# Optimization experiments

Measured on AMD Instinct MI355X. Metric: run time of the kernel, lower is better.

The kernel has to match this reference:

```python
import jax, jax.numpy as jnp
import numpy as np

E = 2048
H = 16
HD = E // H
S = 2048
B = 2
SCALE = 1.0 / np.sqrt(HD)


def setup_inputs() -> dict:
    key = jax.random.key(0)
    ks = jax.random.split(key, 5)
    std = 1.0 / np.sqrt(E)
    return {
        "inX": jax.random.normal(ks[0], (B, S, E), dtype=jnp.float32),
        "W_qkv": jax.random.normal(ks[1], (E, 3 * E), dtype=jnp.float32) * std,
        "b_qkv": jax.random.normal(ks[2], (3 * E,), dtype=jnp.float32) * std,
        "W_out": jax.random.normal(ks[3], (E, E), dtype=jnp.float32) * std,
        "b_out": jax.random.normal(ks[4], (E,), dtype=jnp.float32) * std,
    }


def reference(inX, W_qkv, b_qkv, W_out, b_out):
    b, s, e = inX.shape
    qkv = inX @ W_qkv + b_qkv                      # [B,S,3E]
    q, k, v = jnp.split(qkv, 3, axis=2)
    # [B,S,H,HD] -> [B,H,S,HD]
    q = q.reshape(b, s, H, HD).transpose(0, 2, 1, 3)
    k = k.reshape(b, s, H, HD).transpose(0, 2, 1, 3)
    v = v.reshape(b, s, H, HD).transpose(0, 2, 1, 3)
    att = jnp.einsum("bhqd,bhkd->bhqk", q, k) * SCALE
    causal = jnp.tril(jnp.ones((s, s), dtype=bool))
    att = jnp.where(causal, att, -jnp.inf)
    att = jax.nn.softmax(att, axis=-1)
    out = jnp.einsum("bhqk,bhkd->bhqd", att, v)
    out = out.transpose(0, 2, 1, 3).reshape(b, s, e)
    return out @ W_out + b_out
```

## Files before the change

### kernel.cpp

```cpp
#include <hip/hip_runtime.h>


typedef unsigned short u16;
typedef unsigned int   u32;
typedef __attribute__((ext_vector_type(4)))  float f32x4;
typedef __attribute__((ext_vector_type(16))) float f32x16;
typedef __attribute__((ext_vector_type(4)))  unsigned int u32x4;
typedef __attribute__((ext_vector_type(4)))  unsigned short u16x4;
typedef __attribute__((ext_vector_type(8)))  short bf16x8;

#define E_    2048
#define H_    16
#define HD_   128
#define S_    2048
#define B_    2
#define M_    (B_ * S_)
#define N1_   (3 * E_)
static constexpr float SCALE = 0.08838834764831845f;
static constexpr float C2LOG = 0.12752224f;

__device__ __forceinline__ u16 f2bf(float f) {
  union { float f; u32 u; } x; x.f = f;
  u32 r = x.u + 0x7fffu + ((x.u >> 16) & 1u);
  return (u16)(r >> 16);
}
__device__ __forceinline__ float bfhi2f(u32 u) {
  union { u32 u; float f; } x; x.u = u & 0xffff0000u; return x.f;
}
__device__ __forceinline__ float bflo2f(u32 u) {
  union { u32 u; float f; } x; x.u = u << 16; return x.f;
}
__device__ __forceinline__ u32 pk2(float a, float b) {
  return (u32)f2bf(a) | ((u32)f2bf(b) << 16);
}

__global__ __launch_bounds__(256) void cvt_bf16(const float* __restrict__ x,
                                                u16* __restrict__ y, int n) {
  int i = (blockIdx.x * 256 + threadIdx.x) * 8;
  if (i >= n) return;
  f32x4 a = *(const f32x4*)(x + i);
  f32x4 b = *(const f32x4*)(x + i + 4);
  u16x4 u0 = { f2bf(a[0]), f2bf(a[1]), f2bf(a[2]), f2bf(a[3]) };
  u16x4 u1 = { f2bf(b[0]), f2bf(b[1]), f2bf(b[2]), f2bf(b[3]) };
  *(u16x4*)(y + i)     = u0;
  *(u16x4*)(y + i + 4) = u1;
}

__global__ __launch_bounds__(256) void transpose_cvt_f32(const float* __restrict__ W,
                                                         u16* __restrict__ Wt,
                                                         int rows, int cols) {
  __shared__ __align__(16) u16 tile[64][68];
  const int ct = blockIdx.x, rt = blockIdx.y;
  const int tid = threadIdx.x;
  const int seg = tid & 15, r0 = tid >> 4;
  for (int p = 0; p < 4; ++p) {
    int r = r0 + p * 16;
    f32x4 f = *(const f32x4*)&W[(size_t)(rt * 64 + r) * cols + ct * 64 + seg * 4];
    u16x4 u = { f2bf(f[0]), f2bf(f[1]), f2bf(f[2]), f2bf(f[3]) };
    *(u16x4*)&tile[r][seg * 4] = u;
  }
  __syncthreads();
  for (int p = 0; p < 4; ++p) {
    int oc = r0 + p * 16;
    u16x4 u = { tile[seg * 4 + 0][oc], tile[seg * 4 + 1][oc],
                tile[seg * 4 + 2][oc], tile[seg * 4 + 3][oc] };
    *(u16x4*)&Wt[(size_t)(ct * 64 + oc) * rows + rt * 64 + seg * 4] = u;
  }
}

__global__ __launch_bounds__(256) void transpose_v(const u16* __restrict__ qkv,
                                                   u16* __restrict__ vt) {
  __shared__ __align__(16) u16 tile[64][68];
  const int st = blockIdx.x;
  const int ct = blockIdx.y;
  const int tid = threadIdx.x;
  const int seg = tid & 15, r0 = tid >> 4;
  for (int p = 0; p < 4; ++p) {
    int r = r0 + p * 16;
    *(u16x4*)&tile[r][seg * 4] =
        *(const u16x4*)&qkv[(size_t)(st * 64 + r) * N1_ + 2 * E_ + ct * 64 + seg * 4];
  }
  __syncthreads();
  const int b = st >> 5, s0 = (st & 31) * 64;
  const int h = ct >> 1, d0 = (ct & 1) * 64;
  for (int p = 0; p < 4; ++p) {
    int oc = r0 + p * 16;
    u16x4 u = { tile[seg * 4 + 0][oc], tile[seg * 4 + 1][oc],
                tile[seg * 4 + 2][oc], tile[seg * 4 + 3][oc] };
    *(u16x4*)&vt[(size_t)((b * H_ + h) * HD_ + d0 + oc) * S_ + s0 + seg * 4] = u;
  }
}

template<int OUT_F32>
__global__ __launch_bounds__(256) void gemm_bt(const u16* __restrict__ A,
                                               const u16* __restrict__ Bt,
                                               const float* __restrict__ bias,
                                               void* __restrict__ Cp,
                                               int M, int N, int K) {
  const int bn = blockIdx.x, bm = blockIdx.y;
  const int tid = threadIdx.x;
  const int wid = tid >> 6, l = tid & 63;
  const int l15 = l & 15, l4 = l >> 4;
  const int wr = wid >> 1, wc = wid & 1;

  __shared__ __align__(16) u16 As[128 * 32];
  __shared__ __align__(16) u16 Bs[128 * 32];

  f32x4 acc[4][4] = {};

  const int lrow = l >> 2, lseg = l & 3;
  const u16* gA = A + (size_t)(bm * 128 + lrow) * K + lseg * 8;
  const u16* gB = Bt + (size_t)(bn * 128 + lrow) * K + lseg * 8;

  for (int kt = 0; kt < K; kt += 32) {
    for (int i = 0; i < 2; ++i) {
      int ch = wid * 2 + i;
      __builtin_amdgcn_global_load_lds(
          (__attribute__((address_space(1))) const void*)(gA + (size_t)(ch * 16) * K + kt),
          (__attribute__((address_space(3))) void*)(As + ch * 512), 16, 0, 0);
      __builtin_amdgcn_global_load_lds(
          (__attribute__((address_space(1))) const void*)(gB + (size_t)(ch * 16) * K + kt),
          (__attribute__((address_space(3))) void*)(Bs + ch * 512), 16, 0, 0);
    }
    __syncthreads();
    bf16x8 af[4], bfr[4];
    for (int i = 0; i < 4; ++i) {
      af[i]  = *(const bf16x8*)&As[(wr * 64 + i * 16 + l15) * 32 + l4 * 8];
      bfr[i] = *(const bf16x8*)&Bs[(wc * 64 + i * 16 + l15) * 32 + l4 * 8];
    }
    for (int mi = 0; mi < 4; ++mi)
      for (int ni = 0; ni < 4; ++ni)
        acc[mi][ni] = __builtin_amdgcn_mfma_f32_16x16x32_bf16(af[mi], bfr[ni],
                                                              acc[mi][ni], 0, 0, 0);
    __syncthreads();
  }

  for (int ni = 0; ni < 4; ++ni) {
    int col = bn * 128 + wc * 64 + ni * 16 + l15;
    float bs = bias[col];
    for (int mi = 0; mi < 4; ++mi) {
      int row = bm * 128 + wr * 64 + mi * 16 + l4 * 4;
      for (int j = 0; j < 4; ++j) {
        float v = acc[mi][ni][j] + bs;
        if (OUT_F32) ((float*)Cp)[(size_t)(row + j) * N + col] = v;
        else         ((u16*)Cp)[(size_t)(row + j) * N + col] = f2bf(v);
      }
    }
  }
}

__global__ __launch_bounds__(256) void attn3(const u16* __restrict__ qkv,
                                             const u16* __restrict__ vt,
                                             u16* __restrict__ outp) {
  const int i_lin = (int)blockIdx.x + 16 * (int)blockIdx.y;
  const int bh = i_lin & 31;
  const int h8 = i_lin >> 5;
  const int qt = (h8 < 8) ? h8 : 23 - h8;
  const int b = bh >> 4, h = bh & 15;
  const int tid = threadIdx.x;
  const int w = tid >> 6, l = tid & 63;
  const int l31 = l & 31, hi = l >> 5, l15 = l & 15, l4 = l >> 4;

  __shared__ __align__(16) u16 Ks[128 * 128];
  __shared__ __align__(16) u16 Vs[128 * 128];

  const int q_glob = qt * 128 + w * 32 + l31;
  const int qmin_w = qt * 128 + w * 32;
  const int qmax_w = qmin_w + 31;

  bf16x8 qf[8];
  {
    const u16* qrow = qkv + (size_t)(b * S_ + q_glob) * N1_ + h * HD_;
#pragma unroll
    for (int kd = 0; kd < 8; ++kd) {
      u32x4 raw = *(const u32x4*)(qrow + kd * 16 + hi * 8);
      u32x4 o;
#pragma unroll
      for (int j = 0; j < 4; ++j) {
        float flo = bflo2f(raw[j]) * C2LOG;
        float fhi = bfhi2f(raw[j]) * C2LOG;
        o[j] = (u32)f2bf(flo) | ((u32)f2bf(fhi) << 16);
      }
      union { u32x4 u; bf16x8 b; } cv; cv.u = o; qf[kd] = cv.b;
    }
  }

  int slotKe[8];
#pragma unroll
  for (int kd = 0; kd < 8; ++kd) slotKe[kd] = ((2 * kd + hi) ^ l15) * 8;

  f32x16 o0 = {}, o1 = {}, o2 = {}, o3 = {};
  float m_run = -1e30f, lsum = 0.f;

  const int pairs = qt + 1;
  for (int t = 0; t < pairs; ++t) {
    __syncthreads();
#pragma unroll
    for (int i = 0; i < 8; ++i) {
      const int rowbase = i * 16 + w * 4;
      const int r = rowbase + l4;
      const int e = (l15 ^ (r & 15)) * 8;
      __builtin_amdgcn_global_load_lds(
          (__attribute__((address_space(1))) const void*)
              (qkv + (size_t)(b * S_ + t * 128 + r) * N1_ + E_ + h * HD_ + e),
          (__attribute__((address_space(3))) void*)(Ks + rowbase * 128), 16, 0, 0);
      __builtin_amdgcn_global_load_lds(
          (__attribute__((address_space(1))) const void*)
              (vt + (size_t)(bh * HD_ + r) * S_ + t * 128 + e),
          (__attribute__((address_space(3))) void*)(Vs + rowbase * 128), 16, 0, 0);
    }
    asm volatile("s_waitcnt vmcnt(0)");
    __syncthreads();

#pragma unroll
    for (int p = 0; p < 2; ++p) {
      const int kbase = t * 128 + p * 64;
      if (kbase > qmax_w) continue;

      f32x16 sc0 = {}, sc1 = {};
#pragma unroll
      for (int kd = 0; kd < 8; ++kd) {
        bf16x8 ka0 = *(const bf16x8*)(Ks + (size_t)(p * 64 + l31) * 128 + slotKe[kd]);
        bf16x8 ka1 = *(const bf16x8*)(Ks + (size_t)(p * 64 + 32 + l31) * 128 + slotKe[kd]);
        sc0 = __builtin_amdgcn_mfma_f32_32x32x16_bf16(ka0, qf[kd], sc0, 0, 0, 0);
        sc1 = __builtin_amdgcn_mfma_f32_32x32x16_bf16(ka1, qf[kd], sc1, 0, 0, 0);
      }

      if (kbase + 63 > qmin_w) {
#pragma unroll
        for (int r = 0; r < 16; ++r) {
          int k0 = kbase + 8 * (r >> 2) + 4 * hi + (r & 3);
          if (k0 > q_glob)      sc0[r] = -1e30f;
          if (k0 + 32 > q_glob) sc1[r] = -1e30f;
        }
      }

      float tm = -1e30f;
#pragma unroll
      for (int r = 0; r < 16; ++r) tm = fmaxf(tm, fmaxf(sc0[r], sc1[r]));
      tm = fmaxf(tm, __shfl_xor(tm, 32));
      if (tm > m_run + 8.0f) {
        float alpha = exp2f(m_run - tm);
        m_run = tm;
        lsum *= alpha;
#pragma unroll
        for (int r = 0; r < 16; ++r) {
          o0[r] *= alpha; o1[r] *= alpha; o2[r] *= alpha; o3[r] *= alpha;
        }
      }
      float s0 = 0.f, s1 = 0.f;
#pragma unroll
      for (int r = 0; r < 16; ++r) {
        float p0 = exp2f(sc0[r] - m_run); sc0[r] = p0; s0 += p0;
        float p1 = exp2f(sc1[r] - m_run); sc1[r] = p1; s1 += p1;
      }
      lsum += s0 + s1;

      bf16x8 pf[4];
#pragma unroll
      for (int kd = 0; kd < 4; ++kd) {
        const f32x16& scf = (kd < 2) ? sc0 : sc1;
        const int rb = (kd & 1) * 8;
        u32 xa = pk2(scf[rb + 0], scf[rb + 1]);
        u32 ya = pk2(scf[rb + 2], scf[rb + 3]);
        u32 xb = pk2(scf[rb + 4], scf[rb + 5]);
        u32 yb = pk2(scf[rb + 6], scf[rb + 7]);
        u32 sxa = __shfl_xor(xa, 32), sya = __shfl_xor(ya, 32);
        u32 sxb = __shfl_xor(xb, 32), syb = __shfl_xor(yb, 32);
        u32x4 fw;
        fw[0] = hi ? sxb : xa;   fw[1] = hi ? syb : ya;
        fw[2] = hi ? xb  : sxa;  fw[3] = hi ? yb  : sya;
        union { u32x4 u; bf16x8 b; } cv; cv.u = fw; pf[kd] = cv.b;
      }

#pragma unroll
      for (int kd = 0; kd < 4; ++kd) {
        const int vofs = slotKe[kd] ^ (p * 64);
        bf16x8 va0 = *(const bf16x8*)(Vs + (size_t)(0  + l31) * 128 + vofs);
        bf16x8 va1 = *(const bf16x8*)(Vs + (size_t)(32 + l31) * 128 + vofs);
        bf16x8 va2 = *(const bf16x8*)(Vs + (size_t)(64 + l31) * 128 + vofs);
        bf16x8 va3 = *(const bf16x8*)(Vs + (size_t)(96 + l31) * 128 + vofs);
        o0 = __builtin_amdgcn_mfma_f32_32x32x16_bf16(va0, pf[kd], o0, 0, 0, 0);
        o1 = __builtin_amdgcn_mfma_f32_32x32x16_bf16(va1, pf[kd], o1, 0, 0, 0);
        o2 = __builtin_amdgcn_mfma_f32_32x32x16_bf16(va2, pf[kd], o2, 0, 0, 0);
        o3 = __builtin_amdgcn_mfma_f32_32x32x16_bf16(va3, pf[kd], o3, 0, 0, 0);
      }
    }
  }

  lsum += __shfl_xor(lsum, 32);
  const float inv = 1.0f / lsum;
  u16* orow = outp + (size_t)(b * S_ + q_glob) * E_ + h * HD_;
#pragma unroll
  for (int df = 0; df < 4; ++df) {
    const f32x16& oo = (df == 0) ? o0 : (df == 1) ? o1 : (df == 2) ? o2 : o3;
#pragma unroll
    for (int g = 0; g < 4; ++g) {
      int d = 32 * df + 8 * g + 4 * hi;
      u16x4 u = { f2bf(oo[g * 4 + 0] * inv), f2bf(oo[g * 4 + 1] * inv),
                  f2bf(oo[g * 4 + 2] * inv), f2bf(oo[g * 4 + 3] * inv) };
      *(u16x4*)(orow + d) = u;
    }
  }
}

extern "C" void kernel_launch(void* const* d_in, const int* in_sizes, int n_in,
                              void* d_out, int out_size, void* d_ws, size_t ws_size,
                              hipStream_t stream) {
  const float* inX  = (const float*)d_in[0];
  const float* Wqkv = (const float*)d_in[1];
  const float* bqkv = (const float*)d_in[2];
  const float* Wout = (const float*)d_in[3];
  const float* bout = (const float*)d_in[4];

  char* ws = (char*)d_ws;
  u16* Xb   = (u16*)(ws);
  u16* Wqt  = (u16*)(ws + (16u << 20));
  u16* Wot  = (u16*)(ws + (40u << 20));
  u16* QKV  = (u16*)(ws + (48u << 20));
  u16* Vt   = Wqt;
  u16* Attn = Xb;

  cvt_bf16<<<(M_ * E_) / (256 * 8), 256, 0, stream>>>(inX, Xb, M_ * E_);
  transpose_cvt_f32<<<dim3(N1_ / 64, E_ / 64), 256, 0, stream>>>(Wqkv, Wqt, E_, N1_);
  transpose_cvt_f32<<<dim3(E_ / 64, E_ / 64), 256, 0, stream>>>(Wout, Wot, E_, E_);
  gemm_bt<0><<<dim3(N1_ / 128, M_ / 128), 256, 0, stream>>>(Xb, Wqt, bqkv, (void*)QKV,
                                                            M_, N1_, E_);
  transpose_v<<<dim3(M_ / 64, E_ / 64), 256, 0, stream>>>(QKV, Vt);
  attn3<<<dim3(16, 32), 256, 0, stream>>>(QKV, Vt, Attn);
  gemm_bt<1><<<dim3(E_ / 128, M_ / 128), 256, 0, stream>>>(Attn, Wot, bout, d_out,
                                                           M_, E_, E_);
}
```

Measured before the change: 313.0 us.

## Double-buffer GEMM LDS tiles with BK=64 and XOR-swizzled layout

The bf16 GEMM kernel now uses two LDS buffers with a K-tile of 64 and prefetches the next tile through global_load_lds while MFMAs run on the current one, gated by an explicit vmcnt wait. The LDS layout is XOR-swizzled per row so the fragment reads avoid bank conflicts. The aim is to hide global-load latency and halve the number of barriers per K. In exchange, LDS use quadruples to 64KB per block, which may reduce occupancy, and correctness now depends on the hand-written vmcnt count.

```diff
diff --git a/kernel.cpp b/kernel.cpp
--- a/kernel.cpp
+++ b/kernel.cpp
@@ -103,35 +103,57 @@
   const int l15 = l & 15, l4 = l >> 4;
   const int wr = wid >> 1, wc = wid & 1;
 
-  __shared__ __align__(16) u16 As[128 * 32];
-  __shared__ __align__(16) u16 Bs[128 * 32];
+  __shared__ __align__(16) u16 As[2][128 * 64];
+  __shared__ __align__(16) u16 Bs[2][128 * 64];
 
   f32x4 acc[4][4] = {};
 
-  const int lrow = l >> 2, lseg = l & 3;
-  const u16* gA = A + (size_t)(bm * 128 + lrow) * K + lseg * 8;
-  const u16* gB = Bt + (size_t)(bn * 128 + lrow) * K + lseg * 8;
-
-  for (int kt = 0; kt < K; kt += 32) {
-    for (int i = 0; i < 2; ++i) {
-      int ch = wid * 2 + i;
+  const int srow  = l >> 3;
+  const int sslot = (l & 7) ^ srow;
+  const u16* gA = A  + (size_t)(bm * 128 + srow) * K + sslot * 8;
+  const u16* gB = Bt + (size_t)(bn * 128 + srow) * K + sslot * 8;
+
+  auto stage = [&](int buf, int kt) {
+#pragma unroll
+    for (int i = 0; i < 4; ++i) {
+      const int rb = i * 32 + wid * 8;
       __builtin_amdgcn_global_load_lds(
-          (__attribute__((address_space(1))) const void*)(gA + (size_t)(ch * 16) * K + kt),
-          (__attribute__((address_space(3))) void*)(As + ch * 512), 16, 0, 0);
+          (__attribute__((address_space(1))) const void*)(gA + (size_t)rb * K + kt),
+          (__attribute__((address_space(3))) void*)(&As[buf][rb * 64]), 16, 0, 0);
       __builtin_amdgcn_global_load_lds(
-          (__attribute__((address_space(1))) const void*)(gB + (size_t)(ch * 16) * K + kt),
-          (__attribute__((address_space(3))) void*)(Bs + ch * 512), 16, 0, 0);
+          (__attribute__((address_space(1))) const void*)(gB + (size_t)rb * K + kt),
+          (__attribute__((address_space(3))) void*)(&Bs[buf][rb * 64]), 16, 0, 0);
+    }
+  };
+
+  stage(0, 0);
+  const int nk = K >> 6;
+  for (int n = 0; n < nk; ++n) {
+    const int buf = n & 1;
+    if (n + 1 < nk) {
+      stage(buf ^ 1, (n + 1) << 6);
+      asm volatile("s_waitcnt vmcnt(8)" ::: "memory");
+    } else {
+      asm volatile("s_waitcnt vmcnt(0)" ::: "memory");
     }
     __syncthreads();
-    bf16x8 af[4], bfr[4];
-    for (int i = 0; i < 4; ++i) {
-      af[i]  = *(const bf16x8*)&As[(wr * 64 + i * 16 + l15) * 32 + l4 * 8];
-      bfr[i] = *(const bf16x8*)&Bs[(wc * 64 + i * 16 + l15) * 32 + l4 * 8];
-    }
-    for (int mi = 0; mi < 4; ++mi)
-      for (int ni = 0; ni < 4; ++ni)
-        acc[mi][ni] = __builtin_amdgcn_mfma_f32_16x16x32_bf16(af[mi], bfr[ni],
-                                                              acc[mi][ni], 0, 0, 0);
+
+#pragma unroll
+    for (int ks = 0; ks < 2; ++ks) {
+      bf16x8 af[4], bfr[4];
+      const int ph = ((ks * 4 + l4) ^ (l15 & 7)) * 8;
+#pragma unroll
+      for (int i = 0; i < 4; ++i) {
+        af[i]  = *(const bf16x8*)&As[buf][(wr * 64 + i * 16 + l15) * 64 + ph];
+        bfr[i] = *(const bf16x8*)&Bs[buf][(wc * 64 + i * 16 + l15) * 64 + ph];
+      }
+#pragma unroll
+      for (int mi = 0; mi < 4; ++mi)
+#pragma unroll
+        for (int ni = 0; ni < 4; ++ni)
+          acc[mi][ni] = __builtin_amdgcn_mfma_f32_16x16x32_bf16(af[mi], bfr[ni],
+                                                                acc[mi][ni], 0, 0, 0);
+    }
     __syncthreads();
   }
 
```

Measured after the change: 272.7 us. -12.9%, faster.
